# Optimization experiments

Hardware: AMD Instinct MI355X
Metric: run time of the kernel (lower is better)

## Reference

```python
import jax, jax.numpy as jnp
import numpy as np

# ---- static config (matches init_kwargs) ----
B, N, D, FH, FW, C = 2, 6, 48, 16, 44, 80
OGH, OGW, DOWNSAMPLE = 256, 704, 16
D_MIN, D_MAX = 2.0, 58.0
XB = (-51.2, 51.2, 0.4); YB = (-51.2, 51.2, 0.4); ZB = (-10.0, 10.0, 20.0)
NX, NY, NZ = 256, 256, 1  # (ub-lb)/step per bound
DX = jnp.array([XB[2], YB[2], ZB[2]], jnp.float32)
LOWER = jnp.array([XB[0], YB[0], ZB[0]], jnp.float32)  # bx - dx/2


def _frustum():
    # UD depth discretization: d_i = d_min + i*(d_max-d_min)/D
    ds = D_MIN + (D_MAX - D_MIN) / D * np.arange(D, dtype=np.float32)
    ds = np.broadcast_to(ds[:, None, None], (D, FH, FW))
    xs = np.broadcast_to(np.linspace(0, OGW - 1, FW, dtype=np.float32)[None, None, :], (D, FH, FW))
    ys = np.broadcast_to(np.linspace(0, OGH - 1, FH, dtype=np.float32)[None, :, None], (D, FH, FW))
    return jnp.asarray(np.stack([xs, ys, ds], -1))  # [D,FH,FW,3]

FRUSTUM = _frustum()


def setup_inputs() -> dict:
    key = jax.random.key(0)
    k1, k2 = jax.random.split(key)
    x = jax.random.normal(k1, (B, N, D, FH, FW, C), dtype=jnp.float32)
    # camera-to-ego rotation: ego_x = z_cam (fwd), ego_y = -x_cam, ego_z = -y_cam
    R = np.array([[0.0, 0.0, 1.0], [-1.0, 0.0, 0.0], [0.0, -1.0, 0.0]], np.float32)
    rots = jnp.asarray(np.broadcast_to(R, (B, N, 3, 3)).copy())
    trans = 2.0 * jax.random.normal(k2, (B, N, 3), dtype=jnp.float32)
    K = np.array([[500.0, 0.0, OGW / 2.0], [0.0, 500.0, OGH / 2.0], [0.0, 0.0, 1.0]], np.float32)
    intrins = jnp.asarray(np.broadcast_to(K, (B, N, 3, 3)).copy())
    post_rots = jnp.asarray(np.broadcast_to(np.eye(3, dtype=np.float32), (B, N, 3, 3)).copy())
    post_trans = jnp.zeros((B, N, 3), jnp.float32)
    return {"x": x, "rots": rots, "trans": trans, "intrins": intrins,
            "post_rots": post_rots, "post_trans": post_trans}


def _get_geometry(rots, trans, intrins, post_rots, post_trans):
    # frustum -> ego-frame 3D points: [B,N,D,FH,FW,3]
    pts = FRUSTUM[None, None] - post_trans[:, :, None, None, None, :]
    inv_post = jnp.linalg.inv(post_rots)
    pts = jnp.einsum('bnij,bndhwj->bndhwi', inv_post, pts)
    # un-normalize pixel coords by depth
    pts = jnp.concatenate([pts[..., :2] * pts[..., 2:3], pts[..., 2:3]], axis=-1)
    combine = jnp.einsum('bnij,bnjk->bnik', rots, jnp.linalg.inv(intrins))
    pts = jnp.einsum('bnij,bndhwj->bndhwi', combine, pts)
    return pts + trans[:, :, None, None, None, :]


def _voxel_pooling(geom, x):
    Nprime = B * N * D * FH * FW
    xf = x.reshape(Nprime, C)
    # voxel indices; torch .long() truncates toward zero -> astype matches
    gi = ((geom.reshape(Nprime, 3) - LOWER) / DX).astype(jnp.int32)
    batch_ix = jnp.repeat(jnp.arange(B, dtype=jnp.int32), Nprime // B)
    kept = ((gi[:, 0] >= 0) & (gi[:, 0] < NX) &
            (gi[:, 1] >= 0) & (gi[:, 1] < NY) &
            (gi[:, 2] >= 0) & (gi[:, 2] < NZ))
    gi = jnp.where(kept[:, None], gi, 0)
    # flat index into (B, NZ, NY, NX); equivalent aggregation to sort+quickcumsum
    flat = ((batch_ix * NZ + gi[:, 2]) * NY + gi[:, 1]) * NX + gi[:, 0]
    xm = jnp.where(kept[:, None], xf, 0.0)
    pooled = jax.ops.segment_sum(xm, flat, num_segments=B * NZ * NY * NX)
    final = pooled.reshape(B, NZ, NY, NX, C).transpose(0, 4, 1, 2, 3)
    return final  # [B, C, NZ, NY, NX]


def reference(x, rots, trans, intrins, post_rots, post_trans):
    geom = _get_geometry(rots, trans, intrins, post_rots, post_trans)
    return _voxel_pooling(geom, x)
```

## Files before the change

kernel.cpp:

```cpp
#include <hip/hip_runtime.h>


#define NCH       80
#define GRID_HW   65536
#define OUT_PER_B 5242880
#define HSTRIDE   3520
#define PTS_PER_BN 33792
#define NCOLS     25344
#define CAP       16

#define N_ENT_MAX 405504
#define P_BYTES   129761280u
#define NEXT_OFF  129761280u
#define HEAD_OFF  131383296u
#define CNT_OFF   131907584u
#define META_OFF  131907840u
#define WS_NEED   133529856u

__device__ inline void inv3(const double a[9], double inv[9]) {
    double c00 =  a[4]*a[8] - a[5]*a[7];
    double c01 = -(a[3]*a[8] - a[5]*a[6]);
    double c02 =  a[3]*a[7] - a[4]*a[6];
    double det = a[0]*c00 + a[1]*c01 + a[2]*c02;
    double id  = 1.0/det;
    inv[0] = c00*id;
    inv[1] = (a[2]*a[7]-a[1]*a[8])*id;
    inv[2] = (a[1]*a[5]-a[2]*a[4])*id;
    inv[3] = c01*id;
    inv[4] = (a[0]*a[8]-a[2]*a[6])*id;
    inv[5] = (a[2]*a[3]-a[0]*a[5])*id;
    inv[6] = c02*id;
    inv[7] = (a[1]*a[6]-a[0]*a[7])*id;
    inv[8] = (a[0]*a[4]-a[1]*a[3])*id;
}

__device__ inline void prep_bn(const float* __restrict__ rots,
                               const float* __restrict__ trans,
                               const float* __restrict__ intrins,
                               const float* __restrict__ post_rots,
                               const float* __restrict__ post_trans,
                               int bn, double* o) {
    double pr[9], kk[9], rt[9], ipr[9], ik[9];
    #pragma unroll
    for (int i = 0; i < 9; i++) {
        pr[i] = (double)post_rots[bn*9 + i];
        kk[i] = (double)intrins[bn*9 + i];
        rt[i] = (double)rots[bn*9 + i];
    }
    inv3(pr, ipr);
    inv3(kk, ik);
    #pragma unroll
    for (int i = 0; i < 9; i++) o[i] = ipr[i];
    #pragma unroll
    for (int r = 0; r < 3; r++)
        #pragma unroll
        for (int c = 0; c < 3; c++)
            o[9 + r*3 + c] = rt[r*3+0]*ik[0*3+c] + rt[r*3+1]*ik[1*3+c] + rt[r*3+2]*ik[2*3+c];
    #pragma unroll
    for (int i = 0; i < 3; i++) o[18 + i] = (double)post_trans[bn*3 + i];
    #pragma unroll
    for (int i = 0; i < 3; i++) o[21 + i] = (double)trans[bn*3 + i];
}

__global__ void prep_kernel(const float* __restrict__ rots,
                            const float* __restrict__ trans,
                            const float* __restrict__ intrins,
                            const float* __restrict__ post_rots,
                            const float* __restrict__ post_trans,
                            double* __restrict__ tw) {
    int bn = threadIdx.x;
    if (bn >= 12) return;
    prep_bn(rots, trans, intrins, post_rots, post_trans, bn, tw + bn*24);
}

__global__ __launch_bounds__(256) void zero_kernel(float4* __restrict__ p, int n4) {
    int i = blockIdx.x * 256 + threadIdx.x;
    int stride = gridDim.x * 256;
    for (; i < n4; i += stride) p[i] = make_float4(0.f, 0.f, 0.f, 0.f);
}

__global__ __launch_bounds__(256) void init_heads(int4* __restrict__ head4, int* __restrict__ counter) {
    int i = blockIdx.x * 256 + threadIdx.x;
    head4[i] = make_int4(-1, -1, -1, -1);
    if (i == 0) counter[0] = 0;
}

__global__ __launch_bounds__(256) void geom_cols(const float* __restrict__ rots,
                                                 const float* __restrict__ trans,
                                                 const float* __restrict__ intrins,
                                                 const float* __restrict__ post_rots,
                                                 const float* __restrict__ post_trans,
                                                 int* __restrict__ nxt,
                                                 int* __restrict__ head,
                                                 int* __restrict__ counter,
                                                 unsigned* __restrict__ ent_meta) {
    __shared__ double s_t[12 * 24];

    const int tid  = threadIdx.x;
    const int col  = blockIdx.x * 256 + tid;
    const int lane = tid & 63;

    if (tid < 12)
        prep_bn(rots, trans, intrins, post_rots, post_trans, tid, s_t + tid * 24);
    __syncthreads();

    const int slice = col / 44;
    const int w     = col - slice * 44;
    const int bn    = slice / 48;
    const int d     = slice - bn * 48;
    const int b     = bn / 6;
    const double* t = s_t + bn * 24;

    int vox[16];
    {
        const float dsv = __fadd_rn(2.0f, __fmul_rn((float)(56.0 / 48.0), (float)d));
        const float xsv = (w == 43) ? 703.0f : (float)((double)w * (703.0 / 43.0));
        const double px = (double)xsv - t[18];
        #pragma unroll
        for (int h = 0; h < 16; h++) {
            float ysv = (float)(h * 17);
            double py = (double)ysv - t[19];
            double pz = (double)dsv - t[20];
            double q0 = t[0]*px + t[1]*py + t[2]*pz;
            double q1 = t[3]*px + t[4]*py + t[5]*pz;
            double q2 = t[6]*px + t[7]*py + t[8]*pz;
            q0 *= q2;
            q1 *= q2;
            double e0 = t[9]*q0  + t[10]*q1 + t[11]*q2 + t[21];
            double e1 = t[12]*q0 + t[13]*q1 + t[14]*q2 + t[22];
            double e2 = t[15]*q0 + t[16]*q1 + t[17]*q2 + t[23];
            const double lxy = (double)(-51.2f);
            const double dxy = (double)(0.4f);
            int gx = (int)((e0 - lxy) / dxy);
            int gy = (int)((e1 - lxy) / dxy);
            int gz = (int)((e2 - (double)(-10.0f)) / (double)(20.0f));
            vox[h] = (gx >= 0 && gx < 256 && gy >= 0 && gy < 256 && gz == 0)
                   ? ((b << 16) | (gy << 8) | gx) : -1;
        }
    }

    int cnt = 0;
    #pragma unroll
    for (int h = 0; h < 16; h++) {
        int prev = (h == 0) ? -1 : vox[h - 1];
        if (vox[h] >= 0 && vox[h] != prev) cnt++;
    }

    int pre = cnt;
    #pragma unroll
    for (int off = 1; off < 64; off <<= 1) {
        int n = __shfl_up(pre, off);
        if (lane >= off) pre += n;
    }
    int wtot  = __shfl(pre, 63);
    int wbase = 0;
    if (wtot > 0) {
        if (lane == 63) wbase = atomicAdd(counter, wtot);
        wbase = __shfl(wbase, 63);
    }
    int e = wbase + pre - cnt;

    int cur = -1; unsigned mask = 0;
    #pragma unroll
    for (int h = 0; h < 16; h++) {
        if (vox[h] < 0) {
            if (cur >= 0) {
                ent_meta[e] = ((unsigned)slice << 22) | ((unsigned)w << 16) | mask;
                nxt[e] = atomicExch(&head[cur], e);
                e++; cur = -1; mask = 0;
            }
        } else if (vox[h] != cur) {
            if (cur >= 0) {
                ent_meta[e] = ((unsigned)slice << 22) | ((unsigned)w << 16) | mask;
                nxt[e] = atomicExch(&head[cur], e);
                e++;
            }
            cur = vox[h]; mask = (1u << h);
        } else {
            mask |= (1u << h);
        }
    }
    if (cur >= 0) {
        ent_meta[e] = ((unsigned)slice << 22) | ((unsigned)w << 16) | mask;
        nxt[e] = atomicExch(&head[cur], e);
    }
}

__global__ __launch_bounds__(256) void reduce_kernel(const float* __restrict__ x,
                                                     const unsigned* __restrict__ ent_meta,
                                                     const int* __restrict__ counter,
                                                     float* __restrict__ P) {
    const int NE = counter[0];
    const int total = NE * 20;
    int i = blockIdx.x * 256 + threadIdx.x;
    const int stride = gridDim.x * 256;
    for (; i < total; i += stride) {
        int e  = i / 20;
        int c4 = i - e * 20;
        unsigned meta = ent_meta[e];
        int slice   = (int)(meta >> 22);
        int w       = (int)((meta >> 16) & 63u);
        unsigned mm = meta & 0xFFFFu;
        const float* xb = x + (size_t)(slice * 704 + w) * NCH + c4 * 4;
        float ax = 0.f, ay = 0.f, az = 0.f, aw = 0.f;
        #pragma unroll
        for (int h = 0; h < 16; h++) {
            float4 v = *(const float4*)(xb + h * HSTRIDE);
            float m = (float)((mm >> h) & 1u);
            ax = fmaf(m, v.x, ax);
            ay = fmaf(m, v.y, ay);
            az = fmaf(m, v.z, az);
            aw = fmaf(m, v.w, aw);
        }
        float4 r; r.x = ax; r.y = ay; r.z = az; r.w = aw;
        *(float4*)(P + (size_t)e * NCH + c4 * 4) = r;
    }
}

__global__ __launch_bounds__(256, 6) void gather_tiled(const float* __restrict__ P,
                                                       const int* __restrict__ nxt,
                                                       const int* __restrict__ head,
                                                       float* __restrict__ out) {
    __shared__ float tile[64 * 81];
    __shared__ int   s_ent[64 * CAP];
    __shared__ int   s_cnt[64];
    __shared__ int   s_ovf[64];

    const int tid = threadIdx.x;
    const int b   = blockIdx.x >> 10;
    const int v0  = (blockIdx.x & 1023) * 64;

    if (tid < 64) {
        int e = head[(b << 16) + v0 + tid];
        int c = 0;
        while (e >= 0 && c < CAP) { s_ent[tid * CAP + c] = e; c++; e = nxt[e]; }
        s_cnt[tid] = c;
        s_ovf[tid] = e;
    }
    __syncthreads();

    #pragma unroll
    for (int i = 0; i < 5; i++) {
        int j  = i * 256 + tid;
        int v  = j / 20;
        int c4 = j - v * 20;
        float ax = 0.f, ay = 0.f, az = 0.f, aw = 0.f;
        const int cnt = s_cnt[v];
        for (int k = 0; k < cnt; k++) {
            const float4 p = *(const float4*)(P + (size_t)s_ent[v * CAP + k] * NCH + c4 * 4);
            ax += p.x; ay += p.y; az += p.z; aw += p.w;
        }
        int e = s_ovf[v];
        while (e >= 0) {
            const float4 p = *(const float4*)(P + (size_t)e * NCH + c4 * 4);
            ax += p.x; ay += p.y; az += p.z; aw += p.w;
            e = nxt[e];
        }
        tile[v * 81 + c4 * 4 + 0] = ax;
        tile[v * 81 + c4 * 4 + 1] = ay;
        tile[v * 81 + c4 * 4 + 2] = az;
        tile[v * 81 + c4 * 4 + 3] = aw;
    }
    __syncthreads();

    float* dst = out + (size_t)b * OUT_PER_B + v0;
    #pragma unroll
    for (int i = 0; i < 20; i++) {
        int k  = i * 256 + tid;
        int c  = k >> 6;
        int lv = k & 63;
        dst[(size_t)c * GRID_HW + lv] = tile[lv * 81 + c];
    }
}

__device__ inline void geom_points(const double* __restrict__ t,
                                   int b, int d, int tid, int* s_base) {
    const float dsv = __fadd_rn(2.0f, __fmul_rn((float)(56.0 / 48.0), (float)d));
    for (int idx = tid; idx < 704; idx += 256) {
        const int h = idx / 44;
        const int w = idx - h * 44;
        float xsv = (w == 43) ? 703.0f : (float)((double)w * (703.0 / 43.0));
        float ysv = (float)(h * 17);
        double px = (double)xsv - t[18];
        double py = (double)ysv - t[19];
        double pz = (double)dsv - t[20];
        double q0 = t[0]*px + t[1]*py + t[2]*pz;
        double q1 = t[3]*px + t[4]*py + t[5]*pz;
        double q2 = t[6]*px + t[7]*py + t[8]*pz;
        q0 *= q2;
        q1 *= q2;
        double e0 = t[9]*q0  + t[10]*q1 + t[11]*q2 + t[21];
        double e1 = t[12]*q0 + t[13]*q1 + t[14]*q2 + t[22];
        double e2 = t[15]*q0 + t[16]*q1 + t[17]*q2 + t[23];
        const double lxy = (double)(-51.2f);
        const double dxy = (double)(0.4f);
        int gx = (int)((e0 - lxy) / dxy);
        int gy = (int)((e1 - lxy) / dxy);
        int gz = (int)((e2 - (double)(-10.0f)) / (double)(20.0f));
        int base = -1;
        if (gx >= 0 && gx < 256 && gy >= 0 && gy < 256 && gz == 0)
            base = (b << 16) | (gy << 8) | gx;
        s_base[idx] = base;
    }
}

__global__ __launch_bounds__(256) void scatter_direct_kernel(const float* __restrict__ x,
                                                             const double* __restrict__ ws,
                                                             float* __restrict__ out) {
    __shared__ int      s_base[704];
    __shared__ int      s_colbase[44];
    __shared__ unsigned s_mask[44];
    __shared__ unsigned s_fb[44];

    const int tid = threadIdx.x;
    const int bn  = blockIdx.x / 48;
    const int d   = blockIdx.x - bn * 48;
    const int b   = bn / 6;
    geom_points(ws + bn * 24, b, d, tid, s_base);
    __syncthreads();

    if (tid < 44) {
        int cb = -1; unsigned mm = 0, fb = 0;
        #pragma unroll
        for (int h = 0; h < 16; h++) {
            int pb = s_base[h * 44 + tid];
            if (pb >= 0) {
                if (cb < 0) cb = pb;
                if (pb == cb) mm |= (1u << h);
                else          fb |= (1u << h);
            }
        }
        s_colbase[tid] = cb;
        s_mask[tid]    = mm;
        s_fb[tid]      = fb;
    }
    __syncthreads();

    const float* xb0 = x + ((size_t)bn * PTS_PER_BN + (size_t)d * 704) * NCH;
    #pragma unroll
    for (int pass = 0; pass < 4; pass++) {
        int item = pass * 256 + tid;
        if (item >= 880) break;
        int w  = item / 20;
        int c4 = item - w * 20;
        unsigned mm = s_mask[w];
        unsigned fb = s_fb[w];
        if (!(mm | fb)) continue;
        const float* xb = xb0 + (size_t)w * NCH + c4 * 4;
        float ax = 0.f, ay = 0.f, az = 0.f, aw = 0.f;
        #pragma unroll
        for (int h = 0; h < 16; h++) {
            if ((mm >> h) & 1u) {
                float4 v = *(const float4*)(xb + h * HSTRIDE);
                ax += v.x; ay += v.y; az += v.z; aw += v.w;
            } else if ((fb >> h) & 1u) {
                float4 v = *(const float4*)(xb + h * HSTRIDE);
                int vb = s_base[h * 44 + w];
                float* o = out + (size_t)(vb >> 16) * OUT_PER_B + (vb & 65535);
                atomicAdd(o + (size_t)(c4*4 + 0) * GRID_HW, v.x);
                atomicAdd(o + (size_t)(c4*4 + 1) * GRID_HW, v.y);
                atomicAdd(o + (size_t)(c4*4 + 2) * GRID_HW, v.z);
                atomicAdd(o + (size_t)(c4*4 + 3) * GRID_HW, v.w);
            }
        }
        if (mm) {
            int vb = s_colbase[w];
            float* o = out + (size_t)(vb >> 16) * OUT_PER_B + (vb & 65535);
            atomicAdd(o + (size_t)(c4*4 + 0) * GRID_HW, ax);
            atomicAdd(o + (size_t)(c4*4 + 1) * GRID_HW, ay);
            atomicAdd(o + (size_t)(c4*4 + 2) * GRID_HW, az);
            atomicAdd(o + (size_t)(c4*4 + 3) * GRID_HW, aw);
        }
    }
}

extern "C" void kernel_launch(void* const* d_in, const int* in_sizes, int n_in,
                              void* d_out, int out_size, void* d_ws, size_t ws_size,
                              hipStream_t stream) {
    const float* x          = (const float*)d_in[0];
    const float* rots       = (const float*)d_in[1];
    const float* trans      = (const float*)d_in[2];
    const float* intrins    = (const float*)d_in[3];
    const float* post_rots  = (const float*)d_in[4];
    const float* post_trans = (const float*)d_in[5];
    float* out = (float*)d_out;

    if (ws_size >= (size_t)WS_NEED) {
        float*    P       = (float*)d_ws;
        int*      nxt     = (int*)((char*)d_ws + NEXT_OFF);
        int*      head    = (int*)((char*)d_ws + HEAD_OFF);
        int*      counter = (int*)((char*)d_ws + CNT_OFF);
        unsigned* meta    = (unsigned*)((char*)d_ws + META_OFF);
        init_heads<<<128, 256, 0, stream>>>((int4*)head, counter);
        geom_cols<<<99, 256, 0, stream>>>(rots, trans, intrins,
                                          post_rots, post_trans,
                                          nxt, head, counter, meta);
        reduce_kernel<<<1024, 256, 0, stream>>>(x, meta, counter, P);
        gather_tiled<<<2048, 256, 0, stream>>>(P, nxt, head, out);
    } else if (ws_size >= 12 * 24 * sizeof(double)) {
        double* tw = (double*)d_ws;
        zero_kernel<<<2560, 256, 0, stream>>>((float4*)out, out_size / 16);
        prep_kernel<<<1, 64, 0, stream>>>(rots, trans, intrins, post_rots, post_trans, tw);
        scatter_direct_kernel<<<576, 256, 0, stream>>>(x, tw, out);
    }
}
```

Measured before the change: 224.8 us.

## Replace per-voxel linked lists with fixed slot arrays and run-length entries

```diff
diff --git a/kernel.cpp b/kernel.cpp
--- a/kernel.cpp
+++ b/kernel.cpp
@@ -7,15 +7,16 @@
 #define HSTRIDE   3520
 #define PTS_PER_BN 33792
 #define NCOLS     25344
-#define CAP       16
+#define SLOT_STRIDE 64
 
 #define N_ENT_MAX 405504
-#define P_BYTES   129761280u
-#define NEXT_OFF  129761280u
-#define HEAD_OFF  131383296u
-#define CNT_OFF   131907584u
-#define META_OFF  131907840u
-#define WS_NEED   133529856u
+#define P_BYTES    129761280u
+#define SLOTS_OFF  129761280u
+#define VCNT_OFF   163315712u
+#define CTR_OFF    163840000u
+#define META_OFF   163840256u
+#define OVF_OFF    165462272u
+#define WS_NEED    165986560u
 
 __device__ inline void inv3(const double a[9], double inv[9]) {
     double c00 =  a[4]*a[8] - a[5]*a[7];
@@ -79,10 +80,10 @@
     for (; i < n4; i += stride) p[i] = make_float4(0.f, 0.f, 0.f, 0.f);
 }
 
-__global__ __launch_bounds__(256) void init_heads(int4* __restrict__ head4, int* __restrict__ counter) {
+__global__ __launch_bounds__(256) void init_cnt(int4* __restrict__ vcnt4, int* __restrict__ ctr) {
     int i = blockIdx.x * 256 + threadIdx.x;
-    head4[i] = make_int4(-1, -1, -1, -1);
-    if (i == 0) counter[0] = 0;
+    vcnt4[i] = make_int4(0, 0, 0, 0);
+    if (i == 0) { ctr[0] = 0; ctr[1] = 0; }
 }
 
 __global__ __launch_bounds__(256) void geom_cols(const float* __restrict__ rots,
@@ -90,10 +91,11 @@
                                                  const float* __restrict__ intrins,
                                                  const float* __restrict__ post_rots,
                                                  const float* __restrict__ post_trans,
-                                                 int* __restrict__ nxt,
-                                                 int* __restrict__ head,
-                                                 int* __restrict__ counter,
-                                                 unsigned* __restrict__ ent_meta) {
+                                                 int* __restrict__ slots,
+                                                 int* __restrict__ vcnt,
+                                                 int* __restrict__ ctr,
+                                                 unsigned* __restrict__ ent_meta,
+                                                 int2* __restrict__ ovf) {
     __shared__ double s_t[12 * 24];
 
     const int tid  = threadIdx.x;
@@ -155,88 +157,101 @@
     int wtot  = __shfl(pre, 63);
     int wbase = 0;
     if (wtot > 0) {
-        if (lane == 63) wbase = atomicAdd(counter, wtot);
+        if (lane == 63) wbase = atomicAdd(&ctr[0], wtot);
         wbase = __shfl(wbase, 63);
     }
     int e = wbase + pre - cnt;
 
-    int cur = -1; unsigned mask = 0;
+    int cur = -1; int h0 = 0, len = 0;
     #pragma unroll
     for (int h = 0; h < 16; h++) {
         if (vox[h] < 0) {
             if (cur >= 0) {
-                ent_meta[e] = ((unsigned)slice << 22) | ((unsigned)w << 16) | mask;
-                nxt[e] = atomicExch(&head[cur], e);
-                e++; cur = -1; mask = 0;
+                ent_meta[e] = ((unsigned)slice << 22) | ((unsigned)w << 16)
+                            | ((unsigned)h0 << 5) | (unsigned)len;
+                int idx = atomicAdd(&vcnt[cur], 1);
+                if (idx < SLOT_STRIDE) slots[(size_t)cur * SLOT_STRIDE + idx] = e;
+                else { int o = atomicAdd(&ctr[1], 1); if (o < 65536) ovf[o] = make_int2(cur, e); }
+                e++; cur = -1; len = 0;
             }
         } else if (vox[h] != cur) {
             if (cur >= 0) {
-                ent_meta[e] = ((unsigned)slice << 22) | ((unsigned)w << 16) | mask;
-                nxt[e] = atomicExch(&head[cur], e);
+                ent_meta[e] = ((unsigned)slice << 22) | ((unsigned)w << 16)
+                            | ((unsigned)h0 << 5) | (unsigned)len;
+                int idx = atomicAdd(&vcnt[cur], 1);
+                if (idx < SLOT_STRIDE) slots[(size_t)cur * SLOT_STRIDE + idx] = e;
+                else { int o = atomicAdd(&ctr[1], 1); if (o < 65536) ovf[o] = make_int2(cur, e); }
                 e++;
             }
-            cur = vox[h]; mask = (1u << h);
+            cur = vox[h]; h0 = h; len = 1;
         } else {
-            mask |= (1u << h);
+            len++;
         }
     }
     if (cur >= 0) {
-        ent_meta[e] = ((unsigned)slice << 22) | ((unsigned)w << 16) | mask;
-        nxt[e] = atomicExch(&head[cur], e);
+        ent_meta[e] = ((unsigned)slice << 22) | ((unsigned)w << 16)
+                    | ((unsigned)h0 << 5) | (unsigned)len;
+        int idx = atomicAdd(&vcnt[cur], 1);
+        if (idx < SLOT_STRIDE) slots[(size_t)cur * SLOT_STRIDE + idx] = e;
+        else { int o = atomicAdd(&ctr[1], 1); if (o < 65536) ovf[o] = make_int2(cur, e); }
     }
 }
 
 __global__ __launch_bounds__(256) void reduce_kernel(const float* __restrict__ x,
                                                      const unsigned* __restrict__ ent_meta,
-                                                     const int* __restrict__ counter,
+                                                     const int* __restrict__ ctr,
                                                      float* __restrict__ P) {
-    const int NE = counter[0];
+    const int NE = ctr[0];
     const int total = NE * 20;
     int i = blockIdx.x * 256 + threadIdx.x;
     const int stride = gridDim.x * 256;
     for (; i < total; i += stride) {
         int e  = i / 20;
         int c4 = i - e * 20;
-        unsigned meta = ent_meta[e];
-        int slice   = (int)(meta >> 22);
-        int w       = (int)((meta >> 16) & 63u);
-        unsigned mm = meta & 0xFFFFu;
-        const float* xb = x + (size_t)(slice * 704 + w) * NCH + c4 * 4;
+        unsigned m = ent_meta[e];
+        int slice = (int)(m >> 22);
+        int w     = (int)((m >> 16) & 63u);
+        int h0    = (int)((m >> 5) & 15u);
+        int len   = (int)(m & 31u);
+        const float* xb = x + (size_t)(slice * 704 + w) * NCH
+                            + (size_t)h0 * HSTRIDE + c4 * 4;
         float ax = 0.f, ay = 0.f, az = 0.f, aw = 0.f;
-        #pragma unroll
-        for (int h = 0; h < 16; h++) {
-            float4 v = *(const float4*)(xb + h * HSTRIDE);
-            float m = (float)((mm >> h) & 1u);
-            ax = fmaf(m, v.x, ax);
-            ay = fmaf(m, v.y, ay);
-            az = fmaf(m, v.z, az);
-            aw = fmaf(m, v.w, aw);
+        int hh = 0;
+        for (; hh + 4 <= len; hh += 4) {
+            float4 v0 = *(const float4*)(xb + (size_t)(hh + 0) * HSTRIDE);
+            float4 v1 = *(const float4*)(xb + (size_t)(hh + 1) * HSTRIDE);
+            float4 v2 = *(const float4*)(xb + (size_t)(hh + 2) * HSTRIDE);
+            float4 v3 = *(const float4*)(xb + (size_t)(hh + 3) * HSTRIDE);
+            ax += v0.x; ay += v0.y; az += v0.z; aw += v0.w;
+            ax += v1.x; ay += v1.y; az += v1.z; aw += v1.w;
+            ax += v2.x; ay += v2.y; az += v2.z; aw += v2.w;
+            ax += v3.x; ay += v3.y; az += v3.z; aw += v3.w;
+        }
+        for (; hh < len; hh++) {
+            float4 v = *(const float4*)(xb + (size_t)hh * HSTRIDE);
+            ax += v.x; ay += v.y; az += v.z; aw += v.w;
         }
         float4 r; r.x = ax; r.y = ay; r.z = az; r.w = aw;
         *(float4*)(P + (size_t)e * NCH + c4 * 4) = r;
     }
 }
 
-__global__ __launch_bounds__(256, 6) void gather_tiled(const float* __restrict__ P,
-                                                       const int* __restrict__ nxt,
-                                                       const int* __restrict__ head,
+__global__ __launch_bounds__(256, 6) void gather_slots(const float* __restrict__ P,
+                                                       const int* __restrict__ slots,
+                                                       const int* __restrict__ vcnt,
+                                                       const int* __restrict__ ctr,
+                                                       const int2* __restrict__ ovf,
                                                        float* __restrict__ out) {
     __shared__ float tile[64 * 81];
-    __shared__ int   s_ent[64 * CAP];
     __shared__ int   s_cnt[64];
-    __shared__ int   s_ovf[64];
+    __shared__ int   s_novf;
 
     const int tid = threadIdx.x;
     const int b   = blockIdx.x >> 10;
     const int v0  = (blockIdx.x & 1023) * 64;
 
-    if (tid < 64) {
-        int e = head[(b << 16) + v0 + tid];
-        int c = 0;
-        while (e >= 0 && c < CAP) { s_ent[tid * CAP + c] = e; c++; e = nxt[e]; }
-        s_cnt[tid] = c;
-        s_ovf[tid] = e;
-    }
+    if (tid < 64) s_cnt[tid] = vcnt[(b << 16) + v0 + tid];
+    if (tid == 0) s_novf = ctr[1];
     __syncthreads();
 
     #pragma unroll
@@ -244,17 +259,25 @@
         int j  = i * 256 + tid;
         int v  = j / 20;
         int c4 = j - v * 20;
+        const int vox = (b << 16) + v0 + v;
+        const int cnt = s_cnt[v];
+        const int cl  = (cnt < SLOT_STRIDE) ? cnt : SLOT_STRIDE;
+        const int* sl = slots + (size_t)vox * SLOT_STRIDE;
         float ax = 0.f, ay = 0.f, az = 0.f, aw = 0.f;
-        const int cnt = s_cnt[v];
-        for (int k = 0; k < cnt; k++) {
-            const float4 p = *(const float4*)(P + (size_t)s_ent[v * CAP + k] * NCH + c4 * 4);
-            ax += p.x; ay += p.y; az += p.z; aw += p.w;
-        }
-        int e = s_ovf[v];
-        while (e >= 0) {
+        for (int k = 0; k < cl; k++) {
+            int e = sl[k];
             const float4 p = *(const float4*)(P + (size_t)e * NCH + c4 * 4);
             ax += p.x; ay += p.y; az += p.z; aw += p.w;
-            e = nxt[e];
+        }
+        if (cnt > SLOT_STRIDE) {
+            int no = s_novf; if (no > 65536) no = 65536;
+            for (int j2 = 0; j2 < no; j2++) {
+                int2 pr = ovf[j2];
+                if (pr.x == vox) {
+                    const float4 p = *(const float4*)(P + (size_t)pr.y * NCH + c4 * 4);
+                    ax += p.x; ay += p.y; az += p.z; aw += p.w;
+                }
+            }
         }
         tile[v * 81 + c4 * 4 + 0] = ax;
         tile[v * 81 + c4 * 4 + 1] = ay;
@@ -263,13 +286,17 @@
     }
     __syncthreads();
 
-    float* dst = out + (size_t)b * OUT_PER_B + v0;
-    #pragma unroll
-    for (int i = 0; i < 20; i++) {
-        int k  = i * 256 + tid;
-        int c  = k >> 6;
-        int lv = k & 63;
-        dst[(size_t)c * GRID_HW + lv] = tile[lv * 81 + c];
+    #pragma unroll
+    for (int i = 0; i < 5; i++) {
+        int f   = i * 256 + tid;
+        int c   = f >> 4;
+        int lv4 = f & 15;
+        float4 r;
+        r.x = tile[(lv4 * 4 + 0) * 81 + c];
+        r.y = tile[(lv4 * 4 + 1) * 81 + c];
+        r.z = tile[(lv4 * 4 + 2) * 81 + c];
+        r.w = tile[(lv4 * 4 + 3) * 81 + c];
+        *(float4*)(out + (size_t)b * OUT_PER_B + (size_t)c * GRID_HW + v0 + lv4 * 4) = r;
     }
 }
 
@@ -386,17 +413,18 @@
     float* out = (float*)d_out;
 
     if (ws_size >= (size_t)WS_NEED) {
-        float*    P       = (float*)d_ws;
-        int*      nxt     = (int*)((char*)d_ws + NEXT_OFF);
-        int*      head    = (int*)((char*)d_ws + HEAD_OFF);
-        int*      counter = (int*)((char*)d_ws + CNT_OFF);
-        unsigned* meta    = (unsigned*)((char*)d_ws + META_OFF);
-        init_heads<<<128, 256, 0, stream>>>((int4*)head, counter);
+        float*    P     = (float*)d_ws;
+        int*      slots = (int*)((char*)d_ws + SLOTS_OFF);
+        int*      vcnt  = (int*)((char*)d_ws + VCNT_OFF);
+        int*      ctr   = (int*)((char*)d_ws + CTR_OFF);
+        unsigned* meta  = (unsigned*)((char*)d_ws + META_OFF);
+        int2*     ovf   = (int2*)((char*)d_ws + OVF_OFF);
+        init_cnt<<<128, 256, 0, stream>>>((int4*)vcnt, ctr);
         geom_cols<<<99, 256, 0, stream>>>(rots, trans, intrins,
                                           post_rots, post_trans,
-                                          nxt, head, counter, meta);
-        reduce_kernel<<<1024, 256, 0, stream>>>(x, meta, counter, P);
-        gather_tiled<<<2048, 256, 0, stream>>>(P, nxt, head, out);
+                                          slots, vcnt, ctr, meta, ovf);
+        reduce_kernel<<<1024, 256, 0, stream>>>(x, meta, ctr, P);
+        gather_slots<<<2048, 256, 0, stream>>>(P, slots, vcnt, ctr, ovf, out);
     } else if (ws_size >= 12 * 24 * sizeof(double)) {
         double* tw = (double*)d_ws;
         zero_kernel<<<2560, 256, 0, stream>>>((float4*)out, out_size / 16);
```

Measured after the change: 237.3 us. 1.06x slower.
